# Optimization experiments

Measured on AMD Instinct MI355X. Metric: run time of the kernel, lower is better.

Reference implementation:

```python
import jax, jax.numpy as jnp
import numpy as np
from functools import partial

H = 512          # hidden_size
H4 = H // 4      # goal hidden size
ENC = 8          # enc_steps
DEC = 12         # dec_steps
PRED = 2         # pred_dim (ETH)
B = 512          # batch


def _lin(k, i, o, s=0.05):
    kw, kb = jax.random.split(k)
    return jax.random.normal(kw, (i, o), jnp.float32) * s, jax.random.normal(kb, (o,), jnp.float32) * s


def setup_inputs() -> dict:
    key = jax.random.key(0)
    ks = jax.random.split(key, 32)
    d = {"inputs": jax.random.normal(ks[0], (B, ENC, 6), jnp.float32)}
    d["embed_w"], d["embed_b"] = _lin(ks[1], 6, H)
    d["reg_w"], d["reg_b"] = _lin(ks[2], H, PRED)
    d["ea_w"], d["ea_b"] = _lin(ks[3], H4, 1)
    d["da_w"], d["da_b"] = _lin(ks[4], H4, 1)
    d["e2g_w"], d["e2g_b"] = _lin(ks[5], H, H4)
    d["e2d_w"], d["e2d_b"] = _lin(ks[6], H, H)
    d["gh2i_w"], d["gh2i_b"] = _lin(ks[7], H4, H4)
    d["dh2i_w"], d["dh2i_b"] = _lin(ks[8], H, H)
    d["gh2t_w"], d["gh2t_b"] = _lin(ks[9], H4, H)
    d["g2e_w"], d["g2e_b"] = _lin(ks[10], H4, H4)
    d["g2d_w"], d["g2d_b"] = _lin(ks[11], H4, H4)
    d["enc_wih"], _ = _lin(ks[12], H + H4, 3 * H)
    d["enc_whh"], _ = _lin(ks[13], H, 3 * H)
    d["enc_bih"] = jax.random.normal(ks[14], (3 * H,), jnp.float32) * 0.05
    d["enc_bhh"] = jax.random.normal(ks[15], (3 * H,), jnp.float32) * 0.05
    d["goal_wih"], _ = _lin(ks[16], H4, 3 * H4)
    d["goal_whh"], _ = _lin(ks[17], H4, 3 * H4)
    d["goal_bih"] = jax.random.normal(ks[18], (3 * H4,), jnp.float32) * 0.05
    d["goal_bhh"] = jax.random.normal(ks[19], (3 * H4,), jnp.float32) * 0.05
    d["dec_wih"], _ = _lin(ks[20], H + H4, 3 * H)
    d["dec_whh"], _ = _lin(ks[21], H, 3 * H)
    d["dec_bih"] = jax.random.normal(ks[22], (3 * H,), jnp.float32) * 0.05
    d["dec_bhh"] = jax.random.normal(ks[23], (3 * H,), jnp.float32) * 0.05
    return d


def _gru(x, h, wih, whh, bih, bhh):
    gi = x @ wih + bih          # [B, 3H]
    gh = h @ whh + bhh
    ir, iz, inn = jnp.split(gi, 3, axis=-1)
    hr, hz, hn = jnp.split(gh, 3, axis=-1)
    r = jax.nn.sigmoid(ir + hr)
    z = jax.nn.sigmoid(iz + hz)
    n = jnp.tanh(inn + r * hn)
    return (1.0 - z) * n + z * h


def reference(inputs, embed_w, embed_b, reg_w, reg_b, ea_w, ea_b, da_w, da_b,
              e2g_w, e2g_b, e2d_w, e2d_b, gh2i_w, gh2i_b, dh2i_w, dh2i_b,
              gh2t_w, gh2t_b, g2e_w, g2e_b, g2d_w, g2d_b,
              enc_wih, enc_whh, enc_bih, enc_bhh,
              goal_wih, goal_whh, goal_bih, goal_bhh,
              dec_wih, dec_whh, dec_bih, dec_bhh):
    relu = jax.nn.relu
    b = inputs.shape[0]
    traj_input = relu(inputs @ embed_w + embed_b)           # [B, ENC, H]

    def sge(goal_hidden):
        def gstep(carry, _):
            gh, gi = carry
            gh = _gru(gi, gh, goal_wih, goal_whh, goal_bih, goal_bhh)
            gi = relu(gh @ gh2i_w + gh2i_b)
            return (gh, gi), gh
        gi0 = jnp.zeros((b, H4), traj_input.dtype)
        _, goals = jax.lax.scan(gstep, (goal_hidden, gi0), None, length=DEC)  # [DEC,B,H4]
        goal_traj = relu(goals @ gh2t_w + gh2t_b) @ reg_w + reg_b             # [DEC,B,PRED]
        goal_for_dec = relu(goals @ g2d_w + g2d_b)                            # [DEC,B,H4]
        gfe = relu(goals @ g2e_w + g2e_b).transpose(1, 0, 2)                  # [B,DEC,H4]
        logits = relu(jnp.tanh(gfe) @ ea_w + ea_b)[..., 0]                    # [B,DEC]
        attn = jax.nn.softmax(logits, axis=1)
        goal_for_enc = jnp.einsum('bt,bth->bh', attn, gfe)
        return goal_for_dec, goal_for_enc, goal_traj.transpose(1, 0, 2)

    def decoder(dec_hidden, gfd):
        gfd_b = gfd.transpose(1, 0, 2)  # [B,DEC,H4]
        steps = jnp.arange(DEC)
        def dstep(dh, t):
            mask = (steps >= t)[None, :, None]
            gdi = jnp.where(mask, gfd_b, 0.0)                      # zeros before t, faithful to torch
            logits = relu(jnp.tanh(gdi) @ da_w + da_b)[..., 0]     # [B,DEC]
            attn = jax.nn.softmax(logits, axis=1)
            ctx = jnp.einsum('bt,bth->bh', attn, gdi)
            ddi = relu(dh @ dh2i_w + dh2i_b)
            x = jnp.concatenate([ctx, ddi], axis=-1)
            dh = _gru(x, dh, dec_wih, dec_whh, dec_bih, dec_bhh)
            return dh, dh @ reg_w + reg_b
        _, traj = jax.lax.scan(dstep, dec_hidden, steps)           # [DEC,B,PRED]
        return traj.transpose(1, 0, 2)

    def estep(carry, x_t):
        teh, gfe = carry
        teh = _gru(jnp.concatenate([x_t, gfe], axis=1), teh,
                   enc_wih, enc_whh, enc_bih, enc_bhh)
        goal_hidden = relu(teh @ e2g_w + e2g_b)
        dec_hidden = relu(teh @ e2d_w + e2d_b)
        gfd, gfe, goal_traj = sge(goal_hidden)
        dec_traj = decoder(dec_hidden, gfd)
        return (teh, gfe), (goal_traj, dec_traj)

    teh0 = jnp.zeros((b, H), traj_input.dtype)
    gfe0 = jnp.zeros((b, H4), traj_input.dtype)
    _, (all_goal, all_dec) = jax.lax.scan(estep, (teh0, gfe0),
                                          traj_input.transpose(1, 0, 2))
    # [ENC,B,DEC,PRED] -> [B,ENC,DEC,PRED]
    return all_goal.transpose(1, 0, 2, 3), all_dec.transpose(1, 0, 2, 3)
```

## Files before the change

### kernel.cpp

```cpp
#include <hip/hip_runtime.h>


typedef unsigned short u16;
typedef __attribute__((ext_vector_type(8))) short bf16x8;
typedef __attribute__((ext_vector_type(4))) float f32x4;

static __device__ __forceinline__ float b2f(u16 u) {
  union { float f; unsigned int i; } x; x.i = ((unsigned int)u) << 16; return x.f;
}
static __device__ __forceinline__ u16 f2b(float f) {
  unsigned int u = __float_as_uint(f);
  unsigned int r = (u + 0x7FFFu + ((u >> 16) & 1u)) >> 16;
  return (u16)r;
}
static __device__ __forceinline__ float fsig(float x) {
  return __fdividef(1.f, 1.f + __expf(-x));
}
static __device__ __forceinline__ float ftanh(float x) {
  return 1.f - __fdividef(2.f, __expf(2.f * x) + 1.f);
}
static __device__ __forceinline__ void gload16(const u16* g, u16* l) {
  __builtin_amdgcn_global_load_lds(
      (const __attribute__((address_space(1))) void*)g,
      (__attribute__((address_space(3))) void*)l, 16, 0, 0);
}

struct TransArgs {
  const float* in[13];
  u16* out[13];
  int K[13], N[13], t0[13], nx[13];
};

__global__ __launch_bounds__(256) void transpose_all(TransArgs ta) {
  int bid = blockIdx.x;
  int i = 0;
  for (int k = 1; k < 13; k++) if (bid >= ta.t0[k]) i = k;
  const float* in = ta.in[i];
  u16* out = ta.out[i];
  int K = ta.K[i], N = ta.N[i];
  int local = bid - ta.t0[i];
  int nx = ta.nx[i];
  int tx = local % nx, ty = local / nx;
  __shared__ u16 tbuf[32][33];
  int n0 = tx * 32, k0 = ty * 32;
  int x = threadIdx.x & 31, y = threadIdx.x >> 5;
  for (int q = 0; q < 4; q++) tbuf[y + 8 * q][x] = f2b(in[(size_t)(k0 + y + 8 * q) * N + n0 + x]);
  __syncthreads();
  for (int q = 0; q < 4; q++) out[(size_t)(n0 + y + 8 * q) * K + k0 + x] = tbuf[x][y + 8 * q];
}

__global__ __launch_bounds__(256) void embed_kernel(const float* __restrict__ inp,
                                                    const float* __restrict__ w,
                                                    const float* __restrict__ bias,
                                                    u16* __restrict__ traj) {
  int t = blockIdx.x * 256 + threadIdx.x;
  int h = t & 511, b = (t >> 9) & 511, e = t >> 18;
  float acc = bias[h];
  for (int i = 0; i < 6; i++) acc += inp[(b * 8 + e) * 6 + i] * w[i * 512 + h];
  traj[((e * 512) + b) * 512 + h] = f2b(fmaxf(acc, 0.f));
}

struct GDesc {
  const u16* A; int lda;
  const u16* A2; int lda2; int asplit;
  const u16* W; int ldw;
  const float* bias;
  u16* Cb; int ldc;
  float* Cf;
  u16* Cb2; int ldc2; int route_n;
  int K; int relu; int nblk; int mblk;
};

__global__ __launch_bounds__(256) void gemm128(GDesc d0, GDesc d1) {
  GDesc d = (blockIdx.z == 0) ? d0 : d1;
  if ((int)blockIdx.x >= d.nblk || (int)blockIdx.y >= d.mblk) return;
  __shared__ u16 As[128 * 64];
  __shared__ u16 Bs[128 * 64];
  int tid = threadIdx.x;
  int m0 = blockIdx.y * 128, n0 = blockIdx.x * 128;
  int lane = tid & 63, wave = tid >> 6;
  int wr = wave >> 1, wc = wave & 1;
  int mrow = lane & 15, quad = lane >> 4, kq = quad * 8;
  int rl = lane >> 3;
  int cs = (lane & 7) ^ rl;
  f32x4 acc[4][4] = {};

  for (int k0 = 0; k0 < d.K; k0 += 64) {
    const u16* Asrc; int Alda, kk;
    if (k0 < d.asplit) { Asrc = d.A; Alda = d.lda; kk = k0; }
    else               { Asrc = d.A2; Alda = d.lda2; kk = k0 - d.asplit; }
    __syncthreads();
#pragma unroll
    for (int p = 0; p < 4; p++) {
      int rg = wave * 8 + p * 32;
      int r = rg + rl;
      gload16(&Asrc[(size_t)(m0 + r) * Alda + kk + cs * 8], &As[rg * 64]);
      gload16(&d.W[(size_t)(n0 + r) * d.ldw + k0 + cs * 8], &Bs[rg * 64]);
    }
    __syncthreads();
#pragma unroll
    for (int ks = 0; ks < 2; ks++) {
      bf16x8 af[4], bf[4];
#pragma unroll
      for (int i = 0; i < 4; i++) {
        int ra = wr * 64 + i * 16 + mrow;
        int rb = wc * 64 + i * 16 + mrow;
        af[i] = *(const bf16x8*)&As[ra * 64 + (((ks * 4 + quad) ^ (ra & 7)) * 8)];
        bf[i] = *(const bf16x8*)&Bs[rb * 64 + (((ks * 4 + quad) ^ (rb & 7)) * 8)];
      }
#pragma unroll
      for (int i = 0; i < 4; i++)
#pragma unroll
        for (int j = 0; j < 4; j++)
          acc[i][j] = __builtin_amdgcn_mfma_f32_16x16x32_bf16(af[i], bf[j], acc[i][j], 0, 0, 0);
    }
  }
  int col = lane & 15, rq = (lane >> 4) * 4;
#pragma unroll
  for (int j = 0; j < 4; j++) {
    int n = n0 + wc * 64 + j * 16 + col;
    float bv = d.bias ? d.bias[n] : 0.f;
    bool r2 = (n >= d.route_n);
    u16* cb = r2 ? d.Cb2 : d.Cb;
    int ldc = r2 ? d.ldc2 : d.ldc;
    int nn = r2 ? n - d.route_n : n;
#pragma unroll
    for (int i = 0; i < 4; i++)
#pragma unroll
      for (int r = 0; r < 4; r++) {
        int m = m0 + wr * 64 + i * 16 + rq + r;
        float v = acc[i][j][r] + bv;
        if (d.relu) v = fmaxf(v, 0.f);
        cb[(size_t)m * ldc + nn] = f2b(v);
        if (d.Cf) d.Cf[(size_t)m * d.ldc + n] = v;
      }
  }
}

__global__ __launch_bounds__(256) void gru_pw(const u16* __restrict__ gi,
                                              const u16* __restrict__ gh,
                                              float* __restrict__ hf,
                                              u16* __restrict__ hb, int rows) {
  int t = blockIdx.x * 256 + threadIdx.x;
  if (t >= rows * 64) return;
  int r = t >> 6, j8 = (t & 63) * 8;
  size_t base = (size_t)r * 1536 + j8;
  uint4 ir4 = *(const uint4*)&gi[base];
  uint4 iz4 = *(const uint4*)&gi[base + 512];
  uint4 in4 = *(const uint4*)&gi[base + 1024];
  uint4 hr4 = *(const uint4*)&gh[base];
  uint4 hz4 = *(const uint4*)&gh[base + 512];
  uint4 hn4 = *(const uint4*)&gh[base + 1024];
  const u16* irp = (const u16*)&ir4; const u16* izp = (const u16*)&iz4;
  const u16* inp = (const u16*)&in4; const u16* hrp = (const u16*)&hr4;
  const u16* hzp = (const u16*)&hz4; const u16* hnp = (const u16*)&hn4;
  size_t hoff = (size_t)r * 512 + j8;
  float hv[8];
  *(float4*)&hv[0] = *(const float4*)&hf[hoff];
  *(float4*)&hv[4] = *(const float4*)&hf[hoff + 4];
  u16 hbv[8];
  for (int j = 0; j < 8; j++) {
    float rr = fsig(b2f(irp[j]) + b2f(hrp[j]));
    float zz = fsig(b2f(izp[j]) + b2f(hzp[j]));
    float nn = ftanh(b2f(inp[j]) + rr * b2f(hnp[j]));
    float ho = (1.f - zz) * nn + zz * hv[j];
    hv[j] = ho; hbv[j] = f2b(ho);
  }
  *(float4*)&hf[hoff] = *(const float4*)&hv[0];
  *(float4*)&hf[hoff + 4] = *(const float4*)&hv[4];
  *(uint4*)&hb[hoff] = *(const uint4*)&hbv[0];
}

__global__ __launch_bounds__(256) void head_reg(const u16* __restrict__ goals,
                                                const u16* __restrict__ w_t,
                                                const float* __restrict__ wb,
                                                const float* __restrict__ rw,
                                                const float* __restrict__ rb,
                                                float* __restrict__ out) {
  int tid = threadIdx.x;
  int lane = tid & 63, wave = tid >> 6;
  int rbase = (blockIdx.x * 4 + wave) * 64;
  int mrow = lane & 15, kq = (lane >> 4) * 8;
  int col = lane & 15, rq4 = (lane >> 4) * 4;
  bf16x8 a[4][4];
#pragma unroll
  for (int q = 0; q < 4; q++)
#pragma unroll
    for (int ks = 0; ks < 4; ks++)
      a[q][ks] = *(const bf16x8*)&goals[(size_t)(rbase + q * 16 + mrow) * 128 + ks * 32 + kq];
  float pr0[4][4] = {}, pr1[4][4] = {};
  for (int j = 0; j < 32; j++) {
    bf16x8 b[4];
#pragma unroll
    for (int ks = 0; ks < 4; ks++)
      b[ks] = *(const bf16x8*)&w_t[(size_t)(j * 16 + mrow) * 128 + ks * 32 + kq];
    f32x4 acc[4] = {};
#pragma unroll
    for (int ks = 0; ks < 4; ks++)
#pragma unroll
      for (int q = 0; q < 4; q++)
        acc[q] = __builtin_amdgcn_mfma_f32_16x16x32_bf16(a[q][ks], b[ks], acc[q], 0, 0, 0);
    int n = j * 16 + col;
    float bv = wb[n];
    float rw0 = rw[n * 2], rw1 = rw[n * 2 + 1];
#pragma unroll
    for (int q = 0; q < 4; q++)
#pragma unroll
      for (int r = 0; r < 4; r++) {
        float v = fmaxf(acc[q][r] + bv, 0.f);
        pr0[q][r] += v * rw0;
        pr1[q][r] += v * rw1;
      }
  }
#pragma unroll
  for (int q = 0; q < 4; q++)
#pragma unroll
    for (int r = 0; r < 4; r++)
#pragma unroll
      for (int o = 1; o < 16; o <<= 1) {
        pr0[q][r] += __shfl_xor(pr0[q][r], o);
        pr1[q][r] += __shfl_xor(pr1[q][r], o);
      }
  if (col == 0) {
#pragma unroll
    for (int q = 0; q < 4; q++)
#pragma unroll
      for (int r = 0; r < 4; r++) {
        int m = rbase + q * 16 + rq4 + r;
        int e = m / 6144; int rem = m - e * 6144;
        int t = rem >> 9; int b = rem & 511;
        float* o = out + ((size_t)(b * 8 + e) * 12 + t) * 2;
        o[0] = pr0[q][r] + rb[0];
        o[1] = pr1[q][r] + rb[1];
      }
  }
}

__global__ __launch_bounds__(1024) void gru_dh2i_reg(const u16* __restrict__ gi,
                                                     const u16* __restrict__ gh,
                                                     float* __restrict__ hf,
                                                     u16* __restrict__ hb,
                                                     const u16* __restrict__ w_t,
                                                     const float* __restrict__ wb,
                                                     u16* __restrict__ ddi,
                                                     const float* __restrict__ rw,
                                                     const float* __restrict__ rb,
                                                     float* __restrict__ out, int td) {
  __shared__ u16 dhs[16][520];
  __shared__ u16 dds[16][520];
  int tid = threadIdx.x;
  int lane = tid & 63, wave = tid >> 6;
  int r0 = blockIdx.x * 16;
  {
    int r = r0 + wave;
    int j8 = lane * 8;
    size_t base = (size_t)r * 1536 + j8;
    uint4 ir4 = *(const uint4*)&gi[base];
    uint4 iz4 = *(const uint4*)&gi[base + 512];
    uint4 in4 = *(const uint4*)&gi[base + 1024];
    uint4 hr4 = *(const uint4*)&gh[base];
    uint4 hz4 = *(const uint4*)&gh[base + 512];
    uint4 hn4 = *(const uint4*)&gh[base + 1024];
    const u16* irp = (const u16*)&ir4; const u16* izp = (const u16*)&iz4;
    const u16* inp = (const u16*)&in4; const u16* hrp = (const u16*)&hr4;
    const u16* hzp = (const u16*)&hz4; const u16* hnp = (const u16*)&hn4;
    size_t hoff = (size_t)r * 512 + j8;
    float hv[8];
    *(float4*)&hv[0] = *(const float4*)&hf[hoff];
    *(float4*)&hv[4] = *(const float4*)&hf[hoff + 4];
    u16 hbv[8];
    float p0 = 0.f, p1 = 0.f;
    for (int j = 0; j < 8; j++) {
      float rr = fsig(b2f(irp[j]) + b2f(hrp[j]));
      float zz = fsig(b2f(izp[j]) + b2f(hzp[j]));
      float nn = ftanh(b2f(inp[j]) + rr * b2f(hnp[j]));
      float ho = (1.f - zz) * nn + zz * hv[j];
      hv[j] = ho; hbv[j] = f2b(ho);
      p0 += ho * rw[(j8 + j) * 2];
      p1 += ho * rw[(j8 + j) * 2 + 1];
    }
    *(float4*)&hf[hoff] = *(const float4*)&hv[0];
    *(float4*)&hf[hoff + 4] = *(const float4*)&hv[4];
    *(uint4*)&hb[hoff] = *(const uint4*)&hbv[0];
    *(uint4*)&dhs[wave][j8] = *(const uint4*)&hbv[0];
    for (int o = 32; o; o >>= 1) { p0 += __shfl_down(p0, o); p1 += __shfl_down(p1, o); }
    if (lane == 0) {
      int e = r >> 9, b = r & 511;
      size_t off = ((size_t)(b * 8 + e) * 12 + td) * 2;
      out[off] = p0 + rb[0];
      out[off + 1] = p1 + rb[1];
    }
  }
  __syncthreads();
  int mrow = lane & 15, kq = (lane >> 4) * 8, rq4 = (lane >> 4) * 4;
#pragma unroll
  for (int q = 0; q < 2; q++) {
    int n0 = (wave * 2 + q) * 16;
    f32x4 acc = {};
#pragma unroll
    for (int ks = 0; ks < 16; ks++) {
      bf16x8 a = *(const bf16x8*)&dhs[mrow][ks * 32 + kq];
      bf16x8 bfr = *(const bf16x8*)&w_t[(size_t)(n0 + mrow) * 512 + ks * 32 + kq];
      acc = __builtin_amdgcn_mfma_f32_16x16x32_bf16(a, bfr, acc, 0, 0, 0);
    }
    float bv = wb[n0 + mrow];
#pragma unroll
    for (int x = 0; x < 4; x++)
      dds[rq4 + x][n0 + mrow] = f2b(fmaxf(acc[x] + bv, 0.f));
  }
  __syncthreads();
  int rr = tid >> 6, c8 = (tid & 63) * 8;
  *(uint4*)&ddi[(size_t)(r0 + rr) * 512 + c8] = *(const uint4*)&dds[rr][c8];
}

__global__ __launch_bounds__(512) void goal_mega(const u16* __restrict__ teh,
                                                 const u16* __restrict__ e2g_t,
                                                 const float* __restrict__ e2g_b,
                                                 const u16* __restrict__ wih_t,
                                                 const u16* __restrict__ whh_t,
                                                 const float* __restrict__ bih,
                                                 const float* __restrict__ bhh,
                                                 const u16* __restrict__ g2i_t,
                                                 const float* __restrict__ g2i_b,
                                                 const u16* __restrict__ g2e_t,
                                                 const float* __restrict__ g2e_b,
                                                 const float* __restrict__ eaw,
                                                 const float* __restrict__ eab,
                                                 u16* __restrict__ goals,
                                                 u16* __restrict__ gfe_out) {
  __shared__ u16 ghb[2][16][136];
  __shared__ u16 gib[16][136];
  __shared__ u16 gfe_l[12][16][128];
  __shared__ u16 tehb[16][520];
  int tid = threadIdx.x;
  int r0 = blockIdx.x * 16;
  int lane = tid & 63, wave = tid >> 6;
  int mrow = lane & 15, kq = (lane >> 4) * 8;
  int rq4 = (lane >> 4) * 4;
  int col = lane & 15;
  int ncol = wave * 16 + col;

  for (int idx = tid; idx < 16 * 64; idx += 512) {
    int m = idx >> 6, c8 = (idx & 63) * 8;
    *(uint4*)&tehb[m][c8] = *(const uint4*)&teh[(size_t)(r0 + m) * 512 + c8];
  }
  {
    u16* gz = &gib[0][0];
    for (int idx = tid; idx < 16 * 136; idx += 512) gz[idx] = 0;
  }

  bf16x8 BfI[3][4], BfH[3][4];
  float bI[3], bH[3];
#pragma unroll
  for (int i = 0; i < 3; i++) {
    int n0 = (wave + 8 * i) * 16;
#pragma unroll
    for (int ks = 0; ks < 4; ks++) {
      BfI[i][ks] = *(const bf16x8*)&wih_t[(n0 + mrow) * 128 + ks * 32 + kq];
      BfH[i][ks] = *(const bf16x8*)&whh_t[(n0 + mrow) * 128 + ks * 32 + kq];
    }
    bI[i] = bih[n0 + col];
    bH[i] = bhh[n0 + col];
  }
  bf16x8 GfI[4], GfE[4];
  float bGi, bGe;
  {
    int n0 = wave * 16;
#pragma unroll
    for (int ks = 0; ks < 4; ks++) {
      GfI[ks] = *(const bf16x8*)&g2i_t[(n0 + mrow) * 128 + ks * 32 + kq];
      GfE[ks] = *(const bf16x8*)&g2e_t[(n0 + mrow) * 128 + ks * 32 + kq];
    }
    bGi = g2i_b[n0 + col];
    bGe = g2e_b[n0 + col];
  }
  __syncthreads();

  f32x4 hreg;
  {
    f32x4 a0 = {}, a1 = {};
#pragma unroll
    for (int ks = 0; ks < 8; ks++) {
      bf16x8 x0 = *(const bf16x8*)&tehb[mrow][ks * 32 + kq];
      bf16x8 x1 = *(const bf16x8*)&tehb[mrow][(ks + 8) * 32 + kq];
      bf16x8 w0 = *(const bf16x8*)&e2g_t[(size_t)(wave * 16 + mrow) * 512 + ks * 32 + kq];
      bf16x8 w1 = *(const bf16x8*)&e2g_t[(size_t)(wave * 16 + mrow) * 512 + (ks + 8) * 32 + kq];
      a0 = __builtin_amdgcn_mfma_f32_16x16x32_bf16(x0, w0, a0, 0, 0, 0);
      a1 = __builtin_amdgcn_mfma_f32_16x16x32_bf16(x1, w1, a1, 0, 0, 0);
    }
    float bv = e2g_b[ncol];
#pragma unroll
    for (int r = 0; r < 4; r++) {
      float v = fmaxf(a0[r] + a1[r] + bv, 0.f);
      hreg[r] = v;
      ghb[0][rq4 + r][ncol] = f2b(v);
    }
  }
  __syncthreads();

  for (int t = 0; t < 12; t++) {
    int p = t & 1;
    bf16x8 agi[4], agh[4];
#pragma unroll
    for (int ks = 0; ks < 4; ks++) {
      agi[ks] = *(const bf16x8*)&gib[mrow][ks * 32 + kq];
      agh[ks] = *(const bf16x8*)&ghb[p][mrow][ks * 32 + kq];
    }
    f32x4 gI[3], gH[3];
#pragma unroll
    for (int i = 0; i < 3; i++) {
      f32x4 a1 = {}, a2 = {};
#pragma unroll
      for (int ks = 0; ks < 4; ks++) {
        a1 = __builtin_amdgcn_mfma_f32_16x16x32_bf16(agi[ks], BfI[i][ks], a1, 0, 0, 0);
        a2 = __builtin_amdgcn_mfma_f32_16x16x32_bf16(agh[ks], BfH[i][ks], a2, 0, 0, 0);
      }
      gI[i] = a1; gH[i] = a2;
    }
#pragma unroll
    for (int r = 0; r < 4; r++) {
      float rr = fsig(gI[0][r] + bI[0] + gH[0][r] + bH[0]);
      float zz = fsig(gI[1][r] + bI[1] + gH[1][r] + bH[1]);
      float nn = ftanh(gI[2][r] + bI[2] + rr * (gH[2][r] + bH[2]));
      float ho = (1.f - zz) * nn + zz * hreg[r];
      hreg[r] = ho;
      u16 hb = f2b(ho);
      ghb[1 - p][rq4 + r][ncol] = hb;
      goals[(size_t)(t * 512 + r0 + rq4 + r) * 128 + ncol] = hb;
    }
    __syncthreads();
    bf16x8 ah[4];
#pragma unroll
    for (int ks = 0; ks < 4; ks++)
      ah[ks] = *(const bf16x8*)&ghb[1 - p][mrow][ks * 32 + kq];
    f32x4 ai = {}, ae = {};
#pragma unroll
    for (int ks = 0; ks < 4; ks++) {
      ai = __builtin_amdgcn_mfma_f32_16x16x32_bf16(ah[ks], GfI[ks], ai, 0, 0, 0);
      ae = __builtin_amdgcn_mfma_f32_16x16x32_bf16(ah[ks], GfE[ks], ae, 0, 0, 0);
    }
#pragma unroll
    for (int r = 0; r < 4; r++) {
      gib[rq4 + r][ncol] = f2b(fmaxf(ai[r] + bGi, 0.f));
      gfe_l[t][rq4 + r][ncol] = f2b(fmaxf(ae[r] + bGe, 0.f));
    }
    __syncthreads();
  }

#pragma unroll
  for (int rep = 0; rep < 2; rep++) {
    int m = wave + 8 * rep;
    float w0 = eaw[lane], w1 = eaw[lane + 64];
    float eb = eab[0];
    float v0[12], v1[12], lg[12];
#pragma unroll
    for (int t = 0; t < 12; t++) {
      float a = b2f(gfe_l[t][m][lane]);
      float c = b2f(gfe_l[t][m][lane + 64]);
      v0[t] = a; v1[t] = c;
      float pv = ftanh(a) * w0 + ftanh(c) * w1;
      for (int o = 32; o; o >>= 1) pv += __shfl_xor(pv, o);
      lg[t] = fmaxf(pv + eb, 0.f);
    }
    float mx = lg[0];
#pragma unroll
    for (int t = 1; t < 12; t++) mx = fmaxf(mx, lg[t]);
    float s = 0.f;
#pragma unroll
    for (int t = 0; t < 12; t++) { lg[t] = __expf(lg[t] - mx); s += lg[t]; }
    float inv = __fdividef(1.f, s);
    float c0 = 0.f, c1 = 0.f;
#pragma unroll
    for (int t = 0; t < 12; t++) { c0 += lg[t] * inv * v0[t]; c1 += lg[t] * inv * v1[t]; }
    gfe_out[(r0 + m) * 128 + lane] = f2b(c0);
    gfe_out[(r0 + m) * 128 + lane + 64] = f2b(c1);
  }
}

__global__ __launch_bounds__(256) void attn_ctx_all(const u16* __restrict__ gfd,
                                                    const float* __restrict__ daw,
                                                    const float* __restrict__ dab,
                                                    u16* __restrict__ xctx) {
  int row = (blockIdx.x * 256 + threadIdx.x) >> 6;
  int lane = threadIdx.x & 63;
  int e = row >> 9, b = row & 511;
  float w0 = daw[lane], w1 = daw[lane + 64];
  float bias = dab[0];
  float v0[12], v1[12], lg[12];
#pragma unroll
  for (int s = 0; s < 12; s++) {
    size_t o = ((size_t)(e * 12 + s) * 512 + b) * 128;
    float a = b2f(gfd[o + lane]);
    float c = b2f(gfd[o + 64 + lane]);
    v0[s] = a; v1[s] = c;
    float p = ftanh(a) * w0 + ftanh(c) * w1;
    for (int o2 = 32; o2; o2 >>= 1) p += __shfl_xor(p, o2);
    lg[s] = fmaxf(p + bias, 0.f);
  }
  float base = fmaxf(bias, 0.f);
  float m = base;
#pragma unroll
  for (int s = 0; s < 12; s++) m = fmaxf(m, lg[s]);
  float eb = __expf(base - m);
  float el[12];
#pragma unroll
  for (int s = 0; s < 12; s++) el[s] = __expf(lg[s] - m);
  float S0 = 0.f, S1 = 0.f, sufE = 0.f;
#pragma unroll
  for (int td = 11; td >= 0; td--) {
    sufE += el[td];
    S0 += el[td] * v0[td];
    S1 += el[td] * v1[td];
    float inv = __fdividef(1.f, (float)td * eb + sufE);
    size_t o = ((size_t)td * 4096 + row) * 128;
    xctx[o + lane] = f2b(S0 * inv);
    xctx[o + lane + 64] = f2b(S1 * inv);
  }
}

extern "C" void kernel_launch(void* const* d_in, const int* in_sizes, int n_in,
                              void* d_out, int out_size, void* d_ws, size_t ws_size,
                              hipStream_t stream) {
  const float* inp      = (const float*)d_in[0];
  const float* embed_w  = (const float*)d_in[1];
  const float* embed_b  = (const float*)d_in[2];
  const float* reg_w    = (const float*)d_in[3];
  const float* reg_b    = (const float*)d_in[4];
  const float* ea_w     = (const float*)d_in[5];
  const float* ea_b     = (const float*)d_in[6];
  const float* da_w     = (const float*)d_in[7];
  const float* da_b     = (const float*)d_in[8];
  const float* e2g_w    = (const float*)d_in[9];
  const float* e2g_b    = (const float*)d_in[10];
  const float* e2d_w    = (const float*)d_in[11];
  const float* e2d_b    = (const float*)d_in[12];
  const float* gh2i_w   = (const float*)d_in[13];
  const float* gh2i_b   = (const float*)d_in[14];
  const float* dh2i_w   = (const float*)d_in[15];
  const float* dh2i_b   = (const float*)d_in[16];
  const float* gh2t_w   = (const float*)d_in[17];
  const float* gh2t_b   = (const float*)d_in[18];
  const float* g2e_w    = (const float*)d_in[19];
  const float* g2e_b    = (const float*)d_in[20];
  const float* g2d_w    = (const float*)d_in[21];
  const float* g2d_b    = (const float*)d_in[22];
  const float* enc_wih  = (const float*)d_in[23];
  const float* enc_whh  = (const float*)d_in[24];
  const float* enc_bih  = (const float*)d_in[25];
  const float* enc_bhh  = (const float*)d_in[26];
  const float* goal_wih = (const float*)d_in[27];
  const float* goal_whh = (const float*)d_in[28];
  const float* goal_bih = (const float*)d_in[29];
  const float* goal_bhh = (const float*)d_in[30];
  const float* dec_wih  = (const float*)d_in[31];
  const float* dec_whh  = (const float*)d_in[32];
  const float* dec_bih  = (const float*)d_in[33];
  const float* dec_bhh  = (const float*)d_in[34];

  char* ws = (char*)d_ws;
  size_t off = 0;
  auto alloc = [&](size_t bytes) -> char* {
    char* p = ws + off; off += (bytes + 255) & ~(size_t)255; return p;
  };
  const size_t TSZ = 512 * 512;
  float* teh_f    = (float*)alloc(TSZ * 4);
  u16*   teh_hist = (u16*)  alloc(9 * TSZ * 2);
  u16*   gfe_buf  = (u16*)  alloc(512 * 128 * 2);
  size_t zero_bytes = off;
  u16*   traj     = (u16*)  alloc((size_t)8 * TSZ * 2);
  u16*   goals_all= (u16*)  alloc((size_t)8 * 6144 * 128 * 2);
  u16*   gfd      = (u16*)  alloc((size_t)49152 * 128 * 2);
  u16*   xctx     = (u16*)  alloc((size_t)12 * 4096 * 128 * 2);
  float* dh_f     = (float*)alloc((size_t)4096 * 512 * 4);
  u16*   dh_b     = (u16*)  alloc((size_t)4096 * 512 * 2);
  u16*   ddi      = (u16*)  alloc((size_t)4096 * 512 * 2);
  u16*   giD      = (u16*)  alloc((size_t)4096 * 1536 * 2);
  u16*   ghD      = (u16*)  alloc((size_t)4096 * 1536 * 2);
  u16*   giE = giD, *ghE = ghD;
  u16* enc_wih_t  = (u16*)alloc((size_t)1536 * 640 * 2);
  u16* enc_whh_t  = (u16*)alloc((size_t)1536 * 512 * 2);
  u16* dec_wih_t  = (u16*)alloc((size_t)1536 * 640 * 2);
  u16* dec_whh_t  = (u16*)alloc((size_t)1536 * 512 * 2);
  u16* e2g_t      = (u16*)alloc(128 * 512 * 2);
  u16* e2d_t      = (u16*)alloc(512 * 512 * 2);
  u16* dh2i_t     = (u16*)alloc(512 * 512 * 2);
  u16* head_t     = (u16*)alloc(640 * 128 * 2);
  u16* g2e_t      = (u16*)alloc(128 * 128 * 2);
  u16* goal_wih_t = (u16*)alloc(384 * 128 * 2);
  u16* goal_whh_t = (u16*)alloc(384 * 128 * 2);
  u16* gh2i_t     = (u16*)alloc(128 * 128 * 2);
  if (off > ws_size) return;

  float* out_goal = (float*)d_out;
  float* out_dec  = out_goal + (size_t)512 * 8 * 12 * 2;

  hipMemsetAsync(teh_f, 0, zero_bytes, stream);

  TransArgs ta;
  int ntile = 0, ti = 0;
  auto push = [&](const float* in, u16* out, int K, int N) {
    ta.in[ti] = in; ta.out[ti] = out; ta.K[ti] = K; ta.N[ti] = N;
    ta.t0[ti] = ntile; ta.nx[ti] = N / 32;
    ntile += (K / 32) * (N / 32); ti++;
  };
  push(enc_wih, enc_wih_t, 640, 1536);
  push(enc_whh, enc_whh_t, 512, 1536);
  push(dec_wih, dec_wih_t, 640, 1536);
  push(dec_whh, dec_whh_t, 512, 1536);
  push(e2g_w, e2g_t, 512, 128);
  push(e2d_w, e2d_t, 512, 512);
  push(dh2i_w, dh2i_t, 512, 512);
  push(gh2t_w, head_t, 128, 512);
  push(g2d_w, head_t + 512 * 128, 128, 128);
  push(g2e_w, g2e_t, 128, 128);
  push(goal_wih, goal_wih_t, 128, 384);
  push(goal_whh, goal_whh_t, 128, 384);
  push(gh2i_w, gh2i_t, 128, 128);
  transpose_all<<<ntile, 256, 0, stream>>>(ta);

  embed_kernel<<<8192, 256, 0, stream>>>(inp, embed_w, embed_b, traj);

  const int FAR = 1 << 30;

  for (int e = 0; e < 8; ++e) {
    GDesc dgi{traj + (size_t)e * TSZ, 512, gfe_buf, 128, 512,
              enc_wih_t, 640, enc_bih, giE, 1536, nullptr,
              nullptr, 0, FAR, 640, 0, 12, 4};
    GDesc dgh{teh_hist + (size_t)e * TSZ, 512, nullptr, 0, FAR,
              enc_whh_t, 512, enc_bhh, ghE, 1536, nullptr,
              nullptr, 0, FAR, 512, 0, 12, 4};
    gemm128<<<dim3(12, 4, 2), 256, 0, stream>>>(dgi, dgh);
    gru_pw<<<128, 256, 0, stream>>>(giE, ghE, teh_f, teh_hist + (size_t)(e + 1) * TSZ, 512);
    goal_mega<<<32, 512, 0, stream>>>(teh_hist + (size_t)(e + 1) * TSZ,
                                      e2g_t, e2g_b,
                                      goal_wih_t, goal_whh_t, goal_bih, goal_bhh,
                                      gh2i_t, gh2i_b, g2e_t, g2e_b, ea_w, ea_b,
                                      goals_all + (size_t)e * 6144 * 128, gfe_buf);
  }

  {
    head_reg<<<192, 256, 0, stream>>>(goals_all, head_t, gh2t_b, reg_w, reg_b, out_goal);
    GDesc dg2d{goals_all, 128, nullptr, 0, FAR,
               head_t + 512 * 128, 128, g2d_b, gfd, 128, nullptr,
               nullptr, 0, FAR, 128, 1, 1, 384};
    GDesc de2d{teh_hist + TSZ, 512, nullptr, 0, FAR,
               e2d_t, 512, e2d_b, dh_b, 512, dh_f,
               nullptr, 0, FAR, 512, 1, 4, 32};
    gemm128<<<dim3(4, 384, 2), 256, 0, stream>>>(dg2d, de2d);
    attn_ctx_all<<<1024, 256, 0, stream>>>(gfd, da_w, da_b, xctx);
    GDesc dd0{dh_b, 512, nullptr, 0, FAR,
              dh2i_t, 512, dh2i_b, ddi, 512, nullptr,
              nullptr, 0, FAR, 512, 1, 4, 32};
    gemm128<<<dim3(4, 32, 1), 256, 0, stream>>>(dd0, dd0);
  }

  for (int td = 0; td < 12; ++td) {
    GDesc dgi{xctx + (size_t)td * 4096 * 128, 128, ddi, 512, 128,
              dec_wih_t, 640, dec_bih, giD, 1536, nullptr,
              nullptr, 0, FAR, 640, 0, 12, 32};
    GDesc dgh{dh_b, 512, nullptr, 0, FAR,
              dec_whh_t, 512, dec_bhh, ghD, 1536, nullptr,
              nullptr, 0, FAR, 512, 0, 12, 32};
    gemm128<<<dim3(12, 32, 2), 256, 0, stream>>>(dgi, dgh);
    gru_dh2i_reg<<<256, 1024, 0, stream>>>(giD, ghD, dh_f, dh_b, dh2i_t, dh2i_b, ddi,
                                           reg_w, reg_b, out_dec, td);
  }
}
```

Before: 1.253 ms.

## Hoist encoder input projection out of loop and fuse recurrent GEMM with GRU update

The traj part of the encoder input projection (x @ W_ih[:512]) does not depend on the recurrence, so it is now computed for all 8 steps in one large GEMM that stores fp32 results. Each step then runs one fused kernel that does the h @ W_hh and gfe @ W_ih[512:] MFMA products, adds the precomputed projection and applies the GRU pointwise update. This drops one GEMM launch and one pointwise launch per step, along with the gi/gh bf16 round trips through memory. In exchange the kernel reads weights directly from global memory without LDS tiling, and it adds a large fp32 buffer.

```diff
diff --git a/kernel.cpp b/kernel.cpp
--- a/kernel.cpp
+++ b/kernel.cpp
@@ -137,38 +137,74 @@
   }
 }
 
-__global__ __launch_bounds__(256) void gru_pw(const u16* __restrict__ gi,
-                                              const u16* __restrict__ gh,
-                                              float* __restrict__ hf,
-                                              u16* __restrict__ hb, int rows) {
-  int t = blockIdx.x * 256 + threadIdx.x;
-  if (t >= rows * 64) return;
-  int r = t >> 6, j8 = (t & 63) * 8;
-  size_t base = (size_t)r * 1536 + j8;
-  uint4 ir4 = *(const uint4*)&gi[base];
-  uint4 iz4 = *(const uint4*)&gi[base + 512];
-  uint4 in4 = *(const uint4*)&gi[base + 1024];
-  uint4 hr4 = *(const uint4*)&gh[base];
-  uint4 hz4 = *(const uint4*)&gh[base + 512];
-  uint4 hn4 = *(const uint4*)&gh[base + 1024];
-  const u16* irp = (const u16*)&ir4; const u16* izp = (const u16*)&iz4;
-  const u16* inp = (const u16*)&in4; const u16* hrp = (const u16*)&hr4;
-  const u16* hzp = (const u16*)&hz4; const u16* hnp = (const u16*)&hn4;
-  size_t hoff = (size_t)r * 512 + j8;
-  float hv[8];
-  *(float4*)&hv[0] = *(const float4*)&hf[hoff];
-  *(float4*)&hv[4] = *(const float4*)&hf[hoff + 4];
-  u16 hbv[8];
-  for (int j = 0; j < 8; j++) {
-    float rr = fsig(b2f(irp[j]) + b2f(hrp[j]));
-    float zz = fsig(b2f(izp[j]) + b2f(hzp[j]));
-    float nn = ftanh(b2f(inp[j]) + rr * b2f(hnp[j]));
-    float ho = (1.f - zz) * nn + zz * hv[j];
-    hv[j] = ho; hbv[j] = f2b(ho);
-  }
-  *(float4*)&hf[hoff] = *(const float4*)&hv[0];
-  *(float4*)&hf[hoff + 4] = *(const float4*)&hv[4];
-  *(uint4*)&hb[hoff] = *(const uint4*)&hbv[0];
+__global__ __launch_bounds__(512) void gi_gh_gru(const u16* __restrict__ teh_in,
+                                                 const u16* __restrict__ gfe,
+                                                 const float* __restrict__ gixp_e,
+                                                 const u16* __restrict__ whh_t,
+                                                 const u16* __restrict__ wih_t,
+                                                 const float* __restrict__ bhh,
+                                                 float* __restrict__ hf,
+                                                 u16* __restrict__ teh_out) {
+  __shared__ u16 tehb[16][520];
+  __shared__ u16 gfeb[16][136];
+  int tid = threadIdx.x;
+  int rg = blockIdx.x >> 2, cb = blockIdx.x & 3;
+  int r0 = rg * 16;
+  int lane = tid & 63, wave = tid >> 6;
+  int mrow = lane & 15, kq = (lane >> 4) * 8, rq4 = (lane >> 4) * 4;
+  int col = lane & 15;
+  int n0 = cb * 128 + wave * 16;
+  int c = n0 + col;
+
+  for (int idx = tid; idx < 16 * 64; idx += 512) {
+    int m = idx >> 6, c8 = (idx & 63) * 8;
+    *(uint4*)&tehb[m][c8] = *(const uint4*)&teh_in[(size_t)(r0 + m) * 512 + c8];
+  }
+  for (int idx = tid; idx < 16 * 16; idx += 512) {
+    int m = idx >> 4, c8 = (idx & 15) * 8;
+    *(uint4*)&gfeb[m][c8] = *(const uint4*)&gfe[(size_t)(r0 + m) * 128 + c8];
+  }
+  __syncthreads();
+
+  const u16* WR = &whh_t[(size_t)(n0 + mrow) * 512];
+  const u16* WZ = &whh_t[(size_t)(512 + n0 + mrow) * 512];
+  const u16* WN = &whh_t[(size_t)(1024 + n0 + mrow) * 512];
+  f32x4 aR = {}, aZ = {}, aN = {};
+#pragma unroll
+  for (int ks = 0; ks < 16; ks++) {
+    bf16x8 a = *(const bf16x8*)&tehb[mrow][ks * 32 + kq];
+    aR = __builtin_amdgcn_mfma_f32_16x16x32_bf16(a, *(const bf16x8*)&WR[ks * 32 + kq], aR, 0, 0, 0);
+    aZ = __builtin_amdgcn_mfma_f32_16x16x32_bf16(a, *(const bf16x8*)&WZ[ks * 32 + kq], aZ, 0, 0, 0);
+    aN = __builtin_amdgcn_mfma_f32_16x16x32_bf16(a, *(const bf16x8*)&WN[ks * 32 + kq], aN, 0, 0, 0);
+  }
+  const u16* VR = &wih_t[(size_t)(n0 + mrow) * 640 + 512];
+  const u16* VZ = &wih_t[(size_t)(512 + n0 + mrow) * 640 + 512];
+  const u16* VN = &wih_t[(size_t)(1024 + n0 + mrow) * 640 + 512];
+  f32x4 iR = {}, iZ = {}, iN = {};
+#pragma unroll
+  for (int ks = 0; ks < 4; ks++) {
+    bf16x8 a = *(const bf16x8*)&gfeb[mrow][ks * 32 + kq];
+    iR = __builtin_amdgcn_mfma_f32_16x16x32_bf16(a, *(const bf16x8*)&VR[ks * 32 + kq], iR, 0, 0, 0);
+    iZ = __builtin_amdgcn_mfma_f32_16x16x32_bf16(a, *(const bf16x8*)&VZ[ks * 32 + kq], iZ, 0, 0, 0);
+    iN = __builtin_amdgcn_mfma_f32_16x16x32_bf16(a, *(const bf16x8*)&VN[ks * 32 + kq], iN, 0, 0, 0);
+  }
+
+  float bR = bhh[c], bZ = bhh[512 + c], bN = bhh[1024 + c];
+#pragma unroll
+  for (int r = 0; r < 4; r++) {
+    int m = r0 + rq4 + r;
+    size_t gb = (size_t)m * 1536 + c;
+    float giR = gixp_e[gb] + iR[r];
+    float giZ = gixp_e[gb + 512] + iZ[r];
+    float giN = gixp_e[gb + 1024] + iN[r];
+    float rr = fsig(giR + aR[r] + bR);
+    float zz = fsig(giZ + aZ[r] + bZ);
+    float nn = ftanh(giN + rr * (aN[r] + bN));
+    size_t hoff = (size_t)m * 512 + c;
+    float ho = (1.f - zz) * nn + zz * hf[hoff];
+    hf[hoff] = ho;
+    teh_out[hoff] = f2b(ho);
+  }
 }
 
 __global__ __launch_bounds__(256) void head_reg(const u16* __restrict__ goals,
@@ -568,6 +604,7 @@
   u16*   gfe_buf  = (u16*)  alloc(512 * 128 * 2);
   size_t zero_bytes = off;
   u16*   traj     = (u16*)  alloc((size_t)8 * TSZ * 2);
+  float* gixp     = (float*)alloc((size_t)8 * 512 * 1536 * 4);
   u16*   goals_all= (u16*)  alloc((size_t)8 * 6144 * 128 * 2);
   u16*   gfd      = (u16*)  alloc((size_t)49152 * 128 * 2);
   u16*   xctx     = (u16*)  alloc((size_t)12 * 4096 * 128 * 2);
@@ -576,7 +613,6 @@
   u16*   ddi      = (u16*)  alloc((size_t)4096 * 512 * 2);
   u16*   giD      = (u16*)  alloc((size_t)4096 * 1536 * 2);
   u16*   ghD      = (u16*)  alloc((size_t)4096 * 1536 * 2);
-  u16*   giE = giD, *ghE = ghD;
   u16* enc_wih_t  = (u16*)alloc((size_t)1536 * 640 * 2);
   u16* enc_whh_t  = (u16*)alloc((size_t)1536 * 512 * 2);
   u16* dec_wih_t  = (u16*)alloc((size_t)1536 * 640 * 2);
@@ -622,15 +658,18 @@
 
   const int FAR = 1 << 30;
 
+  {
+    GDesc dx{traj, 512, nullptr, 0, FAR,
+             enc_wih_t, 640, enc_bih, ghD, 1536, gixp,
+             nullptr, 0, FAR, 512, 0, 12, 32};
+    gemm128<<<dim3(12, 32, 1), 256, 0, stream>>>(dx, dx);
+  }
+
   for (int e = 0; e < 8; ++e) {
-    GDesc dgi{traj + (size_t)e * TSZ, 512, gfe_buf, 128, 512,
-              enc_wih_t, 640, enc_bih, giE, 1536, nullptr,
-              nullptr, 0, FAR, 640, 0, 12, 4};
-    GDesc dgh{teh_hist + (size_t)e * TSZ, 512, nullptr, 0, FAR,
-              enc_whh_t, 512, enc_bhh, ghE, 1536, nullptr,
-              nullptr, 0, FAR, 512, 0, 12, 4};
-    gemm128<<<dim3(12, 4, 2), 256, 0, stream>>>(dgi, dgh);
-    gru_pw<<<128, 256, 0, stream>>>(giE, ghE, teh_f, teh_hist + (size_t)(e + 1) * TSZ, 512);
+    gi_gh_gru<<<128, 512, 0, stream>>>(teh_hist + (size_t)e * TSZ, gfe_buf,
+                                       gixp + (size_t)e * 512 * 1536,
+                                       enc_whh_t, enc_wih_t, enc_bhh,
+                                       teh_f, teh_hist + (size_t)(e + 1) * TSZ);
     goal_mega<<<32, 512, 0, stream>>>(teh_hist + (size_t)(e + 1) * TSZ,
                                       e2g_t, e2g_b,
                                       goal_wih_t, goal_whh_t, goal_bih, goal_bhh,
```

Measured after the change: 1.255 ms. No clear change (+0.2%).
